# Kernel tuning notes

Measured on AMD Instinct MI355X. Metric: run time of the kernel, lower is better.

The kernel has to match this reference:

```python
import jax, jax.numpy as jnp
import numpy as np

TAYLOR_ORDER = 16      # Taylor terms after scaling (||A_s|| <= 0.5 -> machine precision)
MAX_SQUARINGS = 16     # fixed upper bound on squaring steps (jit-friendly)


def batched_expm(A):
    """Vectorized scaling-and-squaring matrix exponential for A of shape [..., n, n].

    Replaces the original per-item torch.linalg.matrix_exp Python loop with one
    fused batched computation (same math: exp(Q*t)).
    """
    n = A.shape[-1]
    I = jnp.eye(n, dtype=A.dtype)
    # per-matrix infinity norm [...,]
    nrm = jnp.max(jnp.sum(jnp.abs(A), axis=-1), axis=-1)
    # number of squarings so that scaled norm <= 0.5
    s = jnp.clip(jnp.ceil(jnp.log2(jnp.maximum(nrm, 1e-30) / 0.5)), 0.0, float(MAX_SQUARINGS))
    As = A * jnp.exp2(-s)[..., None, None]
    # Taylor series: P = I + As + As^2/2! + ...
    P = jnp.broadcast_to(I, A.shape)
    term = P
    for k in range(1, TAYLOR_ORDER + 1):
        term = jnp.matmul(term, As) / k
        P = P + term
    # undo scaling: square s times (data-dependent count via masked squaring)
    s_b = s[..., None, None]
    for i in range(MAX_SQUARINGS):
        P = jnp.where(s_b > i, jnp.matmul(P, P), P)
    return P


def setup_inputs() -> dict:
    key = jax.random.key(0)
    k1, k2 = jax.random.split(key)
    rate_matrix = jax.random.normal(k1, (64, 32768, 4, 4), dtype=jnp.float32)
    time = jax.random.uniform(k2, (64,), dtype=jnp.float32)
    return {"rate_matrix": rate_matrix, "time": time}


def reference(rate_matrix, time):
    # Qt = rate_matrix[i, j] * time[i], batched over (batch, seq_len)
    Qt = rate_matrix * time[:, None, None, None]
    return batched_expm(Qt)  # [B, S, 4, 4] transition probability matrices
```

## Files before the change

kernel.cpp:

```cpp
#include <hip/hip_runtime.h>
#include <math.h>


constexpr int TAYLOR_N = 10;

__global__ void __launch_bounds__(256) expm4_kernel(
    const float* __restrict__ A,
    const float* __restrict__ tvec,
    float* __restrict__ out,
    int M, int S)
{
    const int m = blockIdx.x * 256 + threadIdx.x;
    if (m >= M) return;

    const float t = tvec[m / S];

    float a[16];
    const float4* Ap = reinterpret_cast<const float4*>(A) + (size_t)m * 4;
    #pragma unroll
    for (int i = 0; i < 4; ++i) {
        float4 v = Ap[i];
        a[4*i+0] = v.x * t;
        a[4*i+1] = v.y * t;
        a[4*i+2] = v.z * t;
        a[4*i+3] = v.w * t;
    }

    float nrm = 0.0f;
    #pragma unroll
    for (int i = 0; i < 4; ++i) {
        float rs = fabsf(a[4*i+0]) + fabsf(a[4*i+1])
                 + fabsf(a[4*i+2]) + fabsf(a[4*i+3]);
        nrm = fmaxf(nrm, rs);
    }

    float sf = ceilf(log2f(fmaxf(nrm, 1e-30f) * 2.0f));
    sf = fminf(fmaxf(sf, 0.0f), 16.0f);
    const int   si    = (int)sf;
    const float scale = exp2f(-sf);
    #pragma unroll
    for (int i = 0; i < 16; ++i) a[i] *= scale;

    float P[16], T[16];
    #pragma unroll
    for (int i = 0; i < 16; ++i) { T[i] = a[i]; P[i] = a[i]; }
    P[0] += 1.0f; P[5] += 1.0f; P[10] += 1.0f; P[15] += 1.0f;

    #pragma unroll
    for (int k = 2; k <= TAYLOR_N; ++k) {
        const float rk = 1.0f / (float)k;
        #pragma unroll
        for (int i = 0; i < 4; ++i) {
            const float t0 = T[4*i+0], t1 = T[4*i+1];
            const float t2 = T[4*i+2], t3 = T[4*i+3];
            #pragma unroll
            for (int j = 0; j < 4; ++j) {
                float v = t0*a[j] + t1*a[4+j] + t2*a[8+j] + t3*a[12+j];
                v *= rk;
                T[4*i+j] = v;
                P[4*i+j] += v;
            }
        }
    }

    for (int it = 0; it < si; ++it) {
        float Q[16];
        #pragma unroll
        for (int i = 0; i < 4; ++i) {
            const float p0 = P[4*i+0], p1 = P[4*i+1];
            const float p2 = P[4*i+2], p3 = P[4*i+3];
            #pragma unroll
            for (int j = 0; j < 4; ++j) {
                Q[4*i+j] = p0*P[j] + p1*P[4+j] + p2*P[8+j] + p3*P[12+j];
            }
        }
        #pragma unroll
        for (int i = 0; i < 16; ++i) P[i] = Q[i];
    }

    float4* Op = reinterpret_cast<float4*>(out) + (size_t)m * 4;
    #pragma unroll
    for (int i = 0; i < 4; ++i) {
        float4 v;
        v.x = P[4*i+0]; v.y = P[4*i+1]; v.z = P[4*i+2]; v.w = P[4*i+3];
        Op[i] = v;
    }
}

extern "C" void kernel_launch(void* const* d_in, const int* in_sizes, int n_in,
                              void* d_out, int out_size, void* d_ws, size_t ws_size,
                              hipStream_t stream) {
    const float* A    = (const float*)d_in[0];
    const float* tvec = (const float*)d_in[1];
    float* out        = (float*)d_out;

    const int B = in_sizes[1];
    const int M = in_sizes[0] / 16;
    const int S = M / B;

    const int threads = 256;
    const int blocks  = (M + threads - 1) / threads;
    expm4_kernel<<<blocks, threads, 0, stream>>>(A, tvec, out, M, S);
}
```

Measured before the change: 229.9 us.

## Evaluate Taylor polynomial via Paterson-Stockmeyer with packed float2 FMAs

Replaces the order-10 sequential Taylor loop (9 matrix products) with an order-8 polynomial evaluated Paterson-Stockmeyer style using X^2 and X^3 (4 matrix products). Matrix products use 2-wide float vectors so the compiler can emit packed FP32 FMAs on CDNA. Folding the time scale into the scaling constant removes one multiply pass. Lowering the Taylor order from 10 to 8 slightly reduces accuracy, but the scaled norm stays at or below 0.5.

```diff
diff --git a/kernel.cpp b/kernel.cpp
--- a/kernel.cpp
+++ b/kernel.cpp
@@ -2,7 +2,27 @@
 #include <math.h>
 
 
-constexpr int TAYLOR_N = 10;
+typedef float v2f __attribute__((ext_vector_type(2)));
+
+__device__ __forceinline__ void mm4(const v2f (&Am)[4][2],
+                                    const v2f (&Bm)[4][2],
+                                    v2f (&Cm)[4][2])
+{
+#pragma unroll
+    for (int i = 0; i < 4; ++i) {
+        const float a0 = Am[i][0][0], a1 = Am[i][0][1];
+        const float a2 = Am[i][1][0], a3 = Am[i][1][1];
+#pragma unroll
+        for (int p = 0; p < 2; ++p) {
+            v2f acc = Cm[i][p];
+            acc += a0 * Bm[0][p];
+            acc += a1 * Bm[1][p];
+            acc += a2 * Bm[2][p];
+            acc += a3 * Bm[3][p];
+            Cm[i][p] = acc;
+        }
+    }
+}
 
 __global__ void __launch_bounds__(256) expm4_kernel(
     const float* __restrict__ A,
@@ -15,74 +35,78 @@
 
     const float t = tvec[m / S];
 
-    float a[16];
     const float4* Ap = reinterpret_cast<const float4*>(A) + (size_t)m * 4;
-    #pragma unroll
+    float4 r[4];
+#pragma unroll
+    for (int i = 0; i < 4; ++i) r[i] = Ap[i];
+
+    float nrm = 0.0f;
+#pragma unroll
     for (int i = 0; i < 4; ++i) {
-        float4 v = Ap[i];
-        a[4*i+0] = v.x * t;
-        a[4*i+1] = v.y * t;
-        a[4*i+2] = v.z * t;
-        a[4*i+3] = v.w * t;
+        float rs = fabsf(r[i].x) + fabsf(r[i].y) + fabsf(r[i].z) + fabsf(r[i].w);
+        nrm = fmaxf(nrm, rs);
+    }
+    float sf = ceilf(log2f(fmaxf(t * nrm, 1e-30f) * 2.0f));
+    sf = fminf(fmaxf(sf, 0.0f), 16.0f);
+    const int   si = (int)sf;
+    const float c  = t * ldexpf(1.0f, -si);
+
+    v2f X[4][2];
+#pragma unroll
+    for (int i = 0; i < 4; ++i) {
+        X[i][0][0] = r[i].x * c;  X[i][0][1] = r[i].y * c;
+        X[i][1][0] = r[i].z * c;  X[i][1][1] = r[i].w * c;
     }
 
-    float nrm = 0.0f;
-    #pragma unroll
+    v2f X2[4][2] = {};  mm4(X,  X, X2);
+    v2f X3[4][2] = {};  mm4(X2, X, X3);
+
+    constexpr float c2 = 1.f/2.f,   c3 = 1.f/6.f,    c4 = 1.f/24.f;
+    constexpr float c5 = 1.f/120.f, c6 = 1.f/720.f,  c7 = 1.f/5040.f;
+    constexpr float c8 = 1.f/40320.f;
+
+    v2f B2[4][2];
+#pragma unroll
     for (int i = 0; i < 4; ++i) {
-        float rs = fabsf(a[4*i+0]) + fabsf(a[4*i+1])
-                 + fabsf(a[4*i+2]) + fabsf(a[4*i+3]);
-        nrm = fmaxf(nrm, rs);
+#pragma unroll
+        for (int p = 0; p < 2; ++p) B2[i][p] = c7 * X[i][p] + c8 * X2[i][p];
     }
+    B2[0][0][0] += c6; B2[1][0][1] += c6; B2[2][1][0] += c6; B2[3][1][1] += c6;
 
-    float sf = ceilf(log2f(fmaxf(nrm, 1e-30f) * 2.0f));
-    sf = fminf(fmaxf(sf, 0.0f), 16.0f);
-    const int   si    = (int)sf;
-    const float scale = exp2f(-sf);
-    #pragma unroll
-    for (int i = 0; i < 16; ++i) a[i] *= scale;
+    v2f T1[4][2];
+#pragma unroll
+    for (int i = 0; i < 4; ++i) {
+#pragma unroll
+        for (int p = 0; p < 2; ++p) T1[i][p] = c4 * X[i][p] + c5 * X2[i][p];
+    }
+    T1[0][0][0] += c3; T1[1][0][1] += c3; T1[2][1][0] += c3; T1[3][1][1] += c3;
+    mm4(X3, B2, T1);
 
-    float P[16], T[16];
-    #pragma unroll
-    for (int i = 0; i < 16; ++i) { T[i] = a[i]; P[i] = a[i]; }
-    P[0] += 1.0f; P[5] += 1.0f; P[10] += 1.0f; P[15] += 1.0f;
+    v2f P[4][2];
+#pragma unroll
+    for (int i = 0; i < 4; ++i) {
+#pragma unroll
+        for (int p = 0; p < 2; ++p) P[i][p] = X[i][p] + c2 * X2[i][p];
+    }
+    P[0][0][0] += 1.f; P[1][0][1] += 1.f; P[2][1][0] += 1.f; P[3][1][1] += 1.f;
+    mm4(X3, T1, P);
 
-    #pragma unroll
-    for (int k = 2; k <= TAYLOR_N; ++k) {
-        const float rk = 1.0f / (float)k;
-        #pragma unroll
+    for (int it = 0; it < si; ++it) {
+        v2f Q[4][2] = {};
+        mm4(P, P, Q);
+#pragma unroll
         for (int i = 0; i < 4; ++i) {
-            const float t0 = T[4*i+0], t1 = T[4*i+1];
-            const float t2 = T[4*i+2], t3 = T[4*i+3];
-            #pragma unroll
-            for (int j = 0; j < 4; ++j) {
-                float v = t0*a[j] + t1*a[4+j] + t2*a[8+j] + t3*a[12+j];
-                v *= rk;
-                T[4*i+j] = v;
-                P[4*i+j] += v;
-            }
+            P[i][0] = Q[i][0];
+            P[i][1] = Q[i][1];
         }
     }
 
-    for (int it = 0; it < si; ++it) {
-        float Q[16];
-        #pragma unroll
-        for (int i = 0; i < 4; ++i) {
-            const float p0 = P[4*i+0], p1 = P[4*i+1];
-            const float p2 = P[4*i+2], p3 = P[4*i+3];
-            #pragma unroll
-            for (int j = 0; j < 4; ++j) {
-                Q[4*i+j] = p0*P[j] + p1*P[4+j] + p2*P[8+j] + p3*P[12+j];
-            }
-        }
-        #pragma unroll
-        for (int i = 0; i < 16; ++i) P[i] = Q[i];
-    }
-
     float4* Op = reinterpret_cast<float4*>(out) + (size_t)m * 4;
-    #pragma unroll
+#pragma unroll
     for (int i = 0; i < 4; ++i) {
         float4 v;
-        v.x = P[4*i+0]; v.y = P[4*i+1]; v.z = P[4*i+2]; v.w = P[4*i+3];
+        v.x = P[i][0][0]; v.y = P[i][0][1];
+        v.z = P[i][1][0]; v.w = P[i][1][1];
         Op[i] = v;
     }
 }
```

Result: no change. 232.9 us (+1.3%).
